# Kernel tuning notes

Hardware: AMD Instinct MI355X
Metric: run time of the kernel (lower is better)

Reference implementation:

```python
import jax, jax.numpy as jnp
import numpy as np

EPS = 1e-6
N_HEADS = 16


def _inner(x, y):
    # Lorentzian inner product: -x0*y0 + <x_space, y_space>
    return -x[..., 0] * y[..., 0] + jnp.sum(x[..., 1:] * y[..., 1:], axis=-1)


def _project(x):
    sp = jnp.clip(x[..., 1:], -8.0, 8.0)
    x0 = jnp.sqrt(1.0 + jnp.sum(sp ** 2, axis=-1, keepdims=True) + EPS)
    return jnp.concatenate([x0, sp], axis=-1)


def _exp_map(x, v):
    vx = _inner(v, x)[..., None]
    v_tan = v + vx * x
    v_ns = jnp.maximum(_inner(v_tan, v_tan), 0.0)
    v_n = jnp.minimum(jnp.sqrt(v_ns + EPS)[..., None], 5.0)
    res = jnp.cosh(v_n) * x + jnp.sinh(v_n) * v_tan / (v_n + EPS)
    return _project(res)


def _log_map(x, y):
    y = _project(y)
    xy = jnp.minimum(_inner(x, y)[..., None], -(1.0 + EPS))
    d = jnp.maximum(jnp.arccosh(jnp.maximum(-xy, 1.0 + EPS)), 0.001)
    direc = y + xy * x
    dn = jnp.sqrt(jnp.maximum(_inner(direc, direc), EPS))[..., None]
    return d * direc / (dn + EPS)


def setup_inputs() -> dict:
    key = jax.random.key(0)
    ks = jax.random.split(key, 5)
    B, T, d = 2, 1024, 1024
    x = jax.random.normal(ks[0], (B, T, d), dtype=jnp.float32)
    s = 0.02
    Wq = jax.random.normal(ks[1], (d, d), dtype=jnp.float32) * s
    Wk = jax.random.normal(ks[2], (d, d), dtype=jnp.float32) * s
    Wv = jax.random.normal(ks[3], (d, d), dtype=jnp.float32) * s
    Wo = jax.random.normal(ks[4], (d, d), dtype=jnp.float32) * s
    return {"x": x, "Wq": Wq, "Wk": Wk, "Wv": Wv, "Wo": Wo}


def reference(x, Wq, Wk, Wv, Wo):
    B, T, d = x.shape
    h = N_HEADS
    dh = d // h
    mu = jnp.zeros((d,), dtype=x.dtype).at[0].set(1.0)  # hyperboloid origin

    v = _log_map(mu, x)  # [B, T, d]

    def proj_h(w):
        hh = w.reshape(B, T, h, dh)
        sp = jnp.clip(hh[..., 1:], -5.0, 5.0)
        x0 = jnp.sqrt(1.0 + jnp.sum(sp ** 2, axis=-1, keepdims=True) + EPS)
        return jnp.transpose(jnp.concatenate([x0, sp], axis=-1), (0, 2, 1, 3))  # [B,h,T,dh]

    q = proj_h(v @ Wq.T)
    k = proj_h(v @ Wk.T)
    vv = jnp.transpose((v @ Wv.T).reshape(B, T, h, dh), (0, 2, 1, 3))  # [B,h,T,dh]

    # Lorentzian scores: -q0*k0 + <q_space, k_space>
    sc = (-jnp.einsum("bhqi,bhki->bhqk", q[..., :1], k[..., :1])
          + jnp.einsum("bhqc,bhkc->bhqk", q[..., 1:], k[..., 1:])) / (dh ** 0.5)
    at = jax.nn.softmax(sc, axis=-1)
    out = jnp.einsum("bhqk,bhkc->bhqc", at, vv)
    out = jnp.transpose(out, (0, 2, 1, 3)).reshape(B, T, d)
    return _project(_exp_map(mu, out @ Wo.T))
```

## Files before the change

### kernel.cpp

```cpp
#include <hip/hip_runtime.h>

#define EPSF 1e-6f

typedef __bf16 bf16x8 __attribute__((ext_vector_type(8)));
typedef float f32x4 __attribute__((ext_vector_type(4)));
typedef __attribute__((address_space(3))) unsigned int as3_uint;
typedef __attribute__((address_space(1))) const unsigned int as1_uint;

__device__ __forceinline__ unsigned short f2bf(float f) {
  unsigned int u = __builtin_bit_cast(unsigned int, f);
  u += 0x7fffu + ((u >> 16) & 1u);
  return (unsigned short)(u >> 16);
}
__device__ __forceinline__ float bf2f(unsigned short u) {
  unsigned int v = (unsigned int)u << 16;
  return __builtin_bit_cast(float, v);
}

__global__ __launch_bounds__(256) void prep_and_conv(
    const float* __restrict__ x, const float* __restrict__ Wq,
    const float* __restrict__ Wk, const float* __restrict__ Wv,
    const float* __restrict__ Wo, unsigned short* __restrict__ vbf,
    unsigned short* __restrict__ wqk, unsigned short* __restrict__ wvb,
    unsigned short* __restrict__ wob) {
  int bid = blockIdx.x;
  int tid = threadIdx.x;
  if (bid >= 2048) {
    int t = bid - 2048;
    int y = t >> 10;
    const float* src = (y == 0) ? Wq : (y == 1) ? Wk : (y == 2) ? Wv : Wo;
    unsigned short* dst = (y == 0) ? wqk : (y == 1) ? wqk + 1048576
                          : (y == 2) ? wvb : wob;
    int i = (t & 1023) * 256 + tid;
    f32x4 v = ((const f32x4*)src)[i];
    ushort4 o;
    o.x = f2bf(v[0]); o.y = f2bf(v[1]); o.z = f2bf(v[2]); o.w = f2bf(v[3]);
    ((ushort4*)dst)[i] = o;
    return;
  }
  int row = bid;
  const float* xr = x + (size_t)row * 1024;
  float vals[4];
  float ssq = 0.f;
#pragma unroll
  for (int i = 0; i < 4; ++i) {
    int c = tid + i * 256;
    float t = xr[c];
    if (c == 0) {
      vals[i] = 0.f;
    } else {
      t = fminf(fmaxf(t, -8.f), 8.f);
      vals[i] = t;
      ssq += t * t;
    }
  }
#pragma unroll
  for (int off = 32; off; off >>= 1) ssq += __shfl_xor(ssq, off);
  __shared__ float red[4];
  int wv = tid >> 6;
  if ((tid & 63) == 0) red[wv] = ssq;
  __syncthreads();
  ssq = red[0] + red[1] + red[2] + red[3];

  float y0 = sqrtf(1.f + ssq + EPSF);
  float xy = fminf(-y0, -(1.f + EPSF));
  float mxy = fmaxf(-xy, 1.f + EPSF);
  float dd = fmaxf(acoshf(mxy), 0.001f);
  float d0 = y0 + xy;
  float inn = ssq - d0 * d0;
  float dn = sqrtf(fmaxf(inn, EPSF));
  float inv = dd / (dn + EPSF);

  unsigned short* vr = vbf + (size_t)row * 1024;
#pragma unroll
  for (int i = 0; i < 4; ++i) {
    int c = tid + i * 256;
    float o = (c == 0) ? d0 * inv : vals[i] * inv;
    vr[c] = f2bf(o);
  }
}

__device__ __forceinline__ void gemm128_dbuf(
    const unsigned short* __restrict__ A, const unsigned short* __restrict__ Bw,
    int K, int row0, int col0, unsigned short* As, unsigned short* Bs,
    f32x4 (*acc)[4]) {
  int tid = threadIdx.x;
  int lane = tid & 63, w = tid >> 6;
  int wm = (w >> 1) * 64, wn = (w & 1) * 64;
  int lq = lane & 15, g = lane >> 4;
  const unsigned short* Ag =
      A + (size_t)(row0 + w * 8 + (lane >> 3)) * K + (lane & 7) * 8;
  const unsigned short* Bg =
      Bw + (size_t)(col0 + w * 8 + (lane >> 3)) * K + (lane & 7) * 8;

  auto stage = [&](int buf, int k0) {
#pragma unroll
    for (int it = 0; it < 4; ++it) {
      __builtin_amdgcn_global_load_lds(
          (as1_uint*)(Ag + (size_t)(it * 32) * K + k0),
          (as3_uint*)&As[buf * 8192 + (it * 32 + w * 8) * 64], 16, 0, 0);
      __builtin_amdgcn_global_load_lds(
          (as1_uint*)(Bg + (size_t)(it * 32) * K + k0),
          (as3_uint*)&Bs[buf * 8192 + (it * 32 + w * 8) * 64], 16, 0, 0);
    }
  };

  stage(0, 0);
  int buf = 0;
  for (int k0 = 0; k0 < K; k0 += 64) {
    __syncthreads();
    if (k0 + 64 < K) stage(buf ^ 1, k0 + 64);
#pragma unroll
    for (int ks = 0; ks < 2; ++ks) {
      bf16x8 af[4], bfr[4];
#pragma unroll
      for (int i = 0; i < 4; ++i)
        af[i] = *(const bf16x8*)&As[buf * 8192 + (wm + i * 16 + lq) * 64 + ks * 32 + g * 8];
#pragma unroll
      for (int j = 0; j < 4; ++j)
        bfr[j] = *(const bf16x8*)&Bs[buf * 8192 + (wn + j * 16 + lq) * 64 + ks * 32 + g * 8];
#pragma unroll
      for (int i = 0; i < 4; ++i)
#pragma unroll
        for (int j = 0; j < 4; ++j)
          acc[i][j] =
              __builtin_amdgcn_mfma_f32_16x16x32_bf16(af[i], bfr[j], acc[i][j], 0, 0, 0);
    }
    buf ^= 1;
  }
}

__global__ __launch_bounds__(256) void gemm_qkv(
    const unsigned short* __restrict__ vbf, const unsigned short* __restrict__ wqk,
    const unsigned short* __restrict__ wvb, unsigned short* __restrict__ qb,
    unsigned short* __restrict__ kb, unsigned short* __restrict__ vtb) {
  __shared__ unsigned short As[2 * 8192];
  __shared__ unsigned short Bs[2 * 8192];
  f32x4 acc[4][4] = {};
  int tid = threadIdx.x;
  int lane = tid & 63, w = tid >> 6;
  int wm = (w >> 1) * 64, wn = (w & 1) * 64;
  int lq = lane & 15, g = lane >> 4;
  int bid = blockIdx.x;
  bool isVt = (bid % 3 == 2);

  if (!isVt) {
    int q = bid - (bid + 1) / 3;
    int row0 = (q & 15) * 128, col0 = (q >> 4) * 128;
    gemm128_dbuf(vbf, wqk, 1024, row0, col0, As, Bs, acc);
    int headg = (col0 + wn) >> 6;
    int qmode = (headg < 16) ? 1 : 0;
    unsigned short* dst = qmode ? qb : kb;
    size_t colb = (size_t)(headg & 15) * 64;
    float scale = qmode ? 0.125f : 1.f;
#pragma unroll
    for (int i = 0; i < 4; ++i)
#pragma unroll
      for (int r = 0; r < 4; ++r) {
        float s = 0.f;
#pragma unroll
        for (int j = 0; j < 4; ++j) {
          float vc = fminf(fmaxf(acc[i][j][r], -5.f), 5.f);
          s += (j == 0 && lq == 0) ? 0.f : vc * vc;
        }
        s += __shfl_xor(s, 1);
        s += __shfl_xor(s, 2);
        s += __shfl_xor(s, 4);
        s += __shfl_xor(s, 8);
        float x0 = sqrtf(1.f + s + EPSF);
        int row = row0 + wm + i * 16 + g * 4 + r;
#pragma unroll
        for (int j = 0; j < 4; ++j) {
          float vc = fminf(fmaxf(acc[i][j][r], -5.f), 5.f);
          float o = (j == 0 && lq == 0) ? (qmode ? -x0 : x0) : vc;
          dst[(size_t)row * 1024 + colb + j * 16 + lq] = f2bf(o * scale);
        }
      }
  } else {
    int t = bid / 3;
    int row0 = (t & 7) * 128, col0 = (t >> 3) * 128;
    gemm128_dbuf(wvb, vbf, 1024, row0, col0, As, Bs, acc);
#pragma unroll
    for (int i = 0; i < 4; ++i)
#pragma unroll
      for (int j = 0; j < 4; ++j)
#pragma unroll
        for (int r = 0; r < 4; ++r)
          vtb[(size_t)(row0 + wm + i * 16 + g * 4 + r) * 2048 + col0 + wn + j * 16 + lq] =
              f2bf(acc[i][j][r]);
  }
}

__global__ __launch_bounds__(256) void gemm_wo(
    const unsigned short* __restrict__ A, const unsigned short* __restrict__ Bw,
    unsigned short* __restrict__ C) {
  __shared__ unsigned short As[2 * 8192];
  __shared__ unsigned short Bs[2 * 4096];
  int tid = threadIdx.x;
  int lane = tid & 63, w = tid >> 6;
  int wm = (w >> 1) * 64, wn = (w & 1) * 32;
  int lq = lane & 15, g = lane >> 4;
  int row0 = (blockIdx.x & 15) * 128, col0 = (blockIdx.x >> 4) * 64;
  f32x4 acc[4][2] = {};
  const unsigned short* Ag =
      A + (size_t)(row0 + w * 8 + (lane >> 3)) * 1024 + (lane & 7) * 8;
  const unsigned short* Bg =
      Bw + (size_t)(col0 + w * 8 + (lane >> 3)) * 1024 + (lane & 7) * 8;

  auto stage = [&](int buf, int k0) {
#pragma unroll
    for (int it = 0; it < 4; ++it)
      __builtin_amdgcn_global_load_lds(
          (as1_uint*)(Ag + (size_t)(it * 32) * 1024 + k0),
          (as3_uint*)&As[buf * 8192 + (it * 32 + w * 8) * 64], 16, 0, 0);
#pragma unroll
    for (int it = 0; it < 2; ++it)
      __builtin_amdgcn_global_load_lds(
          (as1_uint*)(Bg + (size_t)(it * 32) * 1024 + k0),
          (as3_uint*)&Bs[buf * 4096 + (it * 32 + w * 8) * 64], 16, 0, 0);
  };

  stage(0, 0);
  int buf = 0;
  for (int k0 = 0; k0 < 1024; k0 += 64) {
    __syncthreads();
    if (k0 + 64 < 1024) stage(buf ^ 1, k0 + 64);
#pragma unroll
    for (int ks = 0; ks < 2; ++ks) {
      bf16x8 af[4], bfr[2];
#pragma unroll
      for (int i = 0; i < 4; ++i)
        af[i] = *(const bf16x8*)&As[buf * 8192 + (wm + i * 16 + lq) * 64 + ks * 32 + g * 8];
#pragma unroll
      for (int j = 0; j < 2; ++j)
        bfr[j] = *(const bf16x8*)&Bs[buf * 4096 + (wn + j * 16 + lq) * 64 + ks * 32 + g * 8];
#pragma unroll
      for (int i = 0; i < 4; ++i)
#pragma unroll
        for (int j = 0; j < 2; ++j)
          acc[i][j] =
              __builtin_amdgcn_mfma_f32_16x16x32_bf16(af[i], bfr[j], acc[i][j], 0, 0, 0);
    }
    buf ^= 1;
  }
#pragma unroll
  for (int i = 0; i < 4; ++i)
#pragma unroll
    for (int j = 0; j < 2; ++j)
#pragma unroll
      for (int r = 0; r < 4; ++r)
        C[(size_t)(row0 + wm + i * 16 + g * 4 + r) * 1024 + col0 + wn + j * 16 + lq] =
            f2bf(acc[i][j][r]);
}

__global__ __launch_bounds__(256) void attn_mfma(
    const unsigned short* __restrict__ Qb, const unsigned short* __restrict__ Kb,
    const unsigned short* __restrict__ Vtb, unsigned short* __restrict__ Obf) {
  __shared__ unsigned short Ks[2][64 * 64];
  __shared__ unsigned short Vs[2][64 * 64];
  __shared__ unsigned short Ps[4 * 16 * 64];
  int tid = threadIdx.x;
  int lane = tid & 63, w = tid >> 6;
  int g = lane >> 4, lq = lane & 15;
  int bid = blockIdx.x;
  int idx = bid >> 3;
  int bh = (bid & 7) * 4 + (idx & 3);
  int qt = idx >> 2;
  int b = bh >> 4, h = bh & 15;

  const unsigned short* qrow =
      Qb + (size_t)(b * 1024 + qt * 64 + w * 16 + lq) * 1024 + h * 64;
  bf16x8 qf0 = *(const bf16x8*)(qrow + g * 8);
  bf16x8 qf1 = *(const bf16x8*)(qrow + 32 + g * 8);

  float mreg = -1e30f, lreg = 0.f;
  f32x4 acc[4] = {};
  unsigned short* Pw = Ps + w * 16 * 64;
  int sx = 8 * (lq & 7);

  const unsigned short* Ksrc = Kb + (size_t)(b * 1024) * 1024 + h * 64;
  const unsigned short* Vsrc = Vtb + (size_t)(h * 64) * 2048 + b * 1024;

  int srow = lane >> 3;
  int scg = (lane & 7) ^ srow;
  const unsigned short* Kp = Ksrc + (size_t)(w * 8 + srow) * 1024 + scg * 8;
  const unsigned short* Vp = Vsrc + (size_t)(w * 8 + srow) * 2048 + scg * 8;

  auto stage = [&](int buf, int kt) {
#pragma unroll
    for (int it = 0; it < 2; ++it) {
      __builtin_amdgcn_global_load_lds(
          (as1_uint*)(Kp + (size_t)(kt * 64 + it * 32) * 1024),
          (as3_uint*)&Ks[buf][(it * 32 + w * 8) * 64], 16, 0, 0);
      __builtin_amdgcn_global_load_lds(
          (as1_uint*)(Vp + (size_t)(it * 32) * 2048 + kt * 64),
          (as3_uint*)&Vs[buf][(it * 32 + w * 8) * 64], 16, 0, 0);
    }
  };

  auto compute = [&](int buf) {
    f32x4 st[4];
    __builtin_amdgcn_s_setprio(1);
#pragma unroll
    for (int i = 0; i < 4; ++i) {
      int ro = i * 16 + lq;
      int rb = ro * 64, xx = 8 * (ro & 7);
      bf16x8 a0 = *(const bf16x8*)&Ks[buf][rb + ((g * 8) ^ xx)];
      bf16x8 a1 = *(const bf16x8*)&Ks[buf][rb + ((32 + g * 8) ^ xx)];
      f32x4 z = {};
      z = __builtin_amdgcn_mfma_f32_16x16x32_bf16(a0, qf0, z, 0, 0, 0);
      st[i] = __builtin_amdgcn_mfma_f32_16x16x32_bf16(a1, qf1, z, 0, 0, 0);
    }
    __builtin_amdgcn_s_setprio(0);
    float pmax = st[0][0];
#pragma unroll
    for (int i = 0; i < 4; ++i)
#pragma unroll
      for (int r = 0; r < 4; ++r) pmax = fmaxf(pmax, st[i][r]);
    pmax = fmaxf(pmax, __shfl_xor(pmax, 16));
    pmax = fmaxf(pmax, __shfl_xor(pmax, 32));
    if (__any(pmax > mreg + 8.f)) {
      float nm = fmaxf(mreg, pmax);
      float sc_ = __expf(mreg - nm);
      mreg = nm;
      lreg *= sc_;
      float scr[4];
#pragma unroll
      for (int r = 0; r < 4; ++r) scr[r] = __shfl(sc_, g * 4 + r);
#pragma unroll
      for (int jj = 0; jj < 4; ++jj)
#pragma unroll
        for (int r = 0; r < 4; ++r) acc[jj][r] *= scr[r];
    }
    float ps = 0.f;
#pragma unroll
    for (int i = 0; i < 4; ++i) {
      ushort4 pq;
      float p0 = __expf(st[i][0] - mreg);
      float p1 = __expf(st[i][1] - mreg);
      float p2 = __expf(st[i][2] - mreg);
      float p3 = __expf(st[i][3] - mreg);
      ps += (p0 + p1) + (p2 + p3);
      pq.x = f2bf(p0); pq.y = f2bf(p1); pq.z = f2bf(p2); pq.w = f2bf(p3);
      *(ushort4*)&Pw[lq * 64 + ((g * 4 + i * 16) ^ sx)] = pq;
    }
    ps += __shfl_xor(ps, 16);
    ps += __shfl_xor(ps, 32);
    lreg += ps;

    __builtin_amdgcn_s_setprio(1);
#pragma unroll
    for (int ks = 0; ks < 2; ++ks) {
      bf16x8 pa = *(const bf16x8*)&Pw[lq * 64 + ((ks * 32 + g * 8) ^ sx)];
#pragma unroll
      for (int jj = 0; jj < 4; ++jj) {
        int vr = 16 * jj + lq;
        bf16x8 vb = *(const bf16x8*)&Vs[buf][vr * 64 + ((ks * 32 + g * 8) ^ (8 * (vr & 7)))];
        acc[jj] = __builtin_amdgcn_mfma_f32_16x16x32_bf16(pa, vb, acc[jj], 0, 0, 0);
      }
    }
    __builtin_amdgcn_s_setprio(0);
  };

  stage(0, 0);
  int buf = 0;
  for (int kt = 0; kt < 16; ++kt) {
    __syncthreads();
    if (kt + 1 < 16) stage(buf ^ 1, kt + 1);
    compute(buf);
    buf ^= 1;
  }

  float linv = 1.f / lreg;
  float ilr[4];
#pragma unroll
  for (int r = 0; r < 4; ++r) ilr[r] = __shfl(linv, g * 4 + r);
  unsigned short* obase =
      Obf + (size_t)(b * 1024 + qt * 64 + w * 16) * 1024 + h * 64;
#pragma unroll
  for (int r = 0; r < 4; ++r)
#pragma unroll
    for (int jj = 0; jj < 4; ++jj)
      obase[(size_t)(g * 4 + r) * 1024 + 16 * jj + lq] = f2bf(acc[jj][r] * ilr[r]);
}

__global__ __launch_bounds__(256) void expmap_project(
    const unsigned short* __restrict__ c2, float* __restrict__ out) {
  int row = blockIdx.x;
  int tid = threadIdx.x;
  const unsigned short* cr = c2 + (size_t)row * 1024;
  float vals[4];
  float ssq = 0.f;
#pragma unroll
  for (int i = 0; i < 4; ++i) {
    int c = tid + i * 256;
    float t = bf2f(cr[c]);
    vals[i] = (c == 0) ? 0.f : t;
    ssq += vals[i] * vals[i];
  }
#pragma unroll
  for (int off = 32; off; off >>= 1) ssq += __shfl_xor(ssq, off);
  __shared__ float red1[4], red2[4];
  int wv = tid >> 6;
  if ((tid & 63) == 0) red1[wv] = ssq;
  __syncthreads();
  ssq = red1[0] + red1[1] + red1[2] + red1[3];
  float vn = fminf(sqrtf(ssq + EPSF), 5.f);
  float bf = sinhf(vn) / (vn + EPSF);
  float s2 = 0.f;
#pragma unroll
  for (int i = 0; i < 4; ++i) {
    float r = fminf(fmaxf(bf * vals[i], -8.f), 8.f);
    vals[i] = r;
    s2 += r * r;
  }
#pragma unroll
  for (int off = 32; off; off >>= 1) s2 += __shfl_xor(s2, off);
  if ((tid & 63) == 0) red2[wv] = s2;
  __syncthreads();
  s2 = red2[0] + red2[1] + red2[2] + red2[3];
  float x0 = sqrtf(1.f + s2 + EPSF);
  float* orow = out + (size_t)row * 1024;
#pragma unroll
  for (int i = 0; i < 4; ++i) {
    int c = tid + i * 256;
    orow[c] = (c == 0) ? x0 : vals[i];
  }
}

extern "C" void kernel_launch(void* const* d_in, const int* in_sizes, int n_in,
                              void* d_out, int out_size, void* d_ws, size_t ws_size,
                              hipStream_t stream) {
  (void)in_sizes; (void)n_in; (void)out_size; (void)ws_size;
  const float* x  = (const float*)d_in[0];
  const float* Wq = (const float*)d_in[1];
  const float* Wk = (const float*)d_in[2];
  const float* Wv = (const float*)d_in[3];
  const float* Wo = (const float*)d_in[4];
  float* out = (float*)d_out;

  char* w = (char*)d_ws;
  unsigned short* vbf = (unsigned short*)w; w += (size_t)2048 * 1024 * 2;
  unsigned short* wqk = (unsigned short*)w; w += (size_t)2048 * 1024 * 2;
  unsigned short* wvb = (unsigned short*)w; w += (size_t)1024 * 1024 * 2;
  unsigned short* wob = (unsigned short*)w; w += (size_t)1024 * 1024 * 2;
  unsigned short* vtb = (unsigned short*)w; w += (size_t)1024 * 2048 * 2;
  unsigned short* qb  = (unsigned short*)w; w += (size_t)2048 * 1024 * 2;
  unsigned short* kb  = (unsigned short*)w; w += (size_t)2048 * 1024 * 2;
  unsigned short* aob = (unsigned short*)w; w += (size_t)2048 * 1024 * 2;
  unsigned short* c2  = (unsigned short*)w; w += (size_t)2048 * 1024 * 2;

  prep_and_conv<<<6144, 256, 0, stream>>>(x, Wq, Wk, Wv, Wo, vbf, wqk, wvb, wob);

  gemm_qkv<<<384, 256, 0, stream>>>(vbf, wqk, wvb, qb, kb, vtb);

  attn_mfma<<<512, 256, 0, stream>>>(qb, kb, vtb, aob);

  gemm_wo<<<256, 256, 0, stream>>>(aob, wob, c2);
  expmap_project<<<2048, 256, 0, stream>>>(c2, out);
}
```

Measured before the change: 84.20 us.

## Rebalance QKV GEMM V-tiles and double attention query tile per block

Measured after the change: 85.83 us. No clear change (+1.9%).

```diff
diff --git a/kernel.cpp b/kernel.cpp
--- a/kernel.cpp
+++ b/kernel.cpp
@@ -136,16 +136,15 @@
     unsigned short* __restrict__ kb, unsigned short* __restrict__ vtb) {
   __shared__ unsigned short As[2 * 8192];
   __shared__ unsigned short Bs[2 * 8192];
-  f32x4 acc[4][4] = {};
   int tid = threadIdx.x;
   int lane = tid & 63, w = tid >> 6;
-  int wm = (w >> 1) * 64, wn = (w & 1) * 64;
   int lq = lane & 15, g = lane >> 4;
   int bid = blockIdx.x;
-  bool isVt = (bid % 3 == 2);
-
-  if (!isVt) {
-    int q = bid - (bid + 1) / 3;
+
+  if ((bid & 1) == 0) {
+    int q = bid >> 1;
+    int wm = (w >> 1) * 64, wn = (w & 1) * 64;
+    f32x4 acc[4][4] = {};
     int row0 = (q & 15) * 128, col0 = (q >> 4) * 128;
     gemm128_dbuf(vbf, wqk, 1024, row0, col0, As, Bs, acc);
     int headg = (col0 + wn) >> 6;
@@ -177,13 +176,53 @@
         }
       }
   } else {
-    int t = bid / 3;
-    int row0 = (t & 7) * 128, col0 = (t >> 3) * 128;
-    gemm128_dbuf(wvb, vbf, 1024, row0, col0, As, Bs, acc);
+    int t = bid >> 1;
+    int wm = (w >> 1) * 64, wn = (w & 1) * 32;
+    int row0 = (t & 7) * 128, col0 = (t >> 3) * 64;
+    f32x4 acc[4][2] = {};
+    const unsigned short* Ag =
+        wvb + (size_t)(row0 + w * 8 + (lane >> 3)) * 1024 + (lane & 7) * 8;
+    const unsigned short* Bg =
+        vbf + (size_t)(col0 + w * 8 + (lane >> 3)) * 1024 + (lane & 7) * 8;
+    auto stage = [&](int buf, int k0) {
+#pragma unroll
+      for (int it = 0; it < 4; ++it)
+        __builtin_amdgcn_global_load_lds(
+            (as1_uint*)(Ag + (size_t)(it * 32) * 1024 + k0),
+            (as3_uint*)&As[buf * 8192 + (it * 32 + w * 8) * 64], 16, 0, 0);
+#pragma unroll
+      for (int it = 0; it < 2; ++it)
+        __builtin_amdgcn_global_load_lds(
+            (as1_uint*)(Bg + (size_t)(it * 32) * 1024 + k0),
+            (as3_uint*)&Bs[buf * 4096 + (it * 32 + w * 8) * 64], 16, 0, 0);
+    };
+    stage(0, 0);
+    int buf = 0;
+    for (int k0 = 0; k0 < 1024; k0 += 64) {
+      __syncthreads();
+      if (k0 + 64 < 1024) stage(buf ^ 1, k0 + 64);
+#pragma unroll
+      for (int ks = 0; ks < 2; ++ks) {
+        bf16x8 af[4], bfr[2];
+#pragma unroll
+        for (int i = 0; i < 4; ++i)
+          af[i] = *(const bf16x8*)&As[buf * 8192 + (wm + i * 16 + lq) * 64 + ks * 32 + g * 8];
+#pragma unroll
+        for (int j = 0; j < 2; ++j)
+          bfr[j] = *(const bf16x8*)&Bs[buf * 4096 + (wn + j * 16 + lq) * 64 + ks * 32 + g * 8];
+#pragma unroll
+        for (int i = 0; i < 4; ++i)
+#pragma unroll
+          for (int j = 0; j < 2; ++j)
+            acc[i][j] =
+                __builtin_amdgcn_mfma_f32_16x16x32_bf16(af[i], bfr[j], acc[i][j], 0, 0, 0);
+      }
+      buf ^= 1;
+    }
 #pragma unroll
     for (int i = 0; i < 4; ++i)
 #pragma unroll
-      for (int j = 0; j < 4; ++j)
+      for (int j = 0; j < 2; ++j)
 #pragma unroll
         for (int r = 0; r < 4; ++r)
           vtb[(size_t)(row0 + wm + i * 16 + g * 4 + r) * 2048 + col0 + wn + j * 16 + lq] =
@@ -253,12 +292,12 @@
             f2bf(acc[i][j][r]);
 }
 
-__global__ __launch_bounds__(256) void attn_mfma(
+__global__ __launch_bounds__(512) void attn_mfma(
     const unsigned short* __restrict__ Qb, const unsigned short* __restrict__ Kb,
     const unsigned short* __restrict__ Vtb, unsigned short* __restrict__ Obf) {
   __shared__ unsigned short Ks[2][64 * 64];
   __shared__ unsigned short Vs[2][64 * 64];
-  __shared__ unsigned short Ps[4 * 16 * 64];
+  __shared__ unsigned short Ps[8 * 16 * 64];
   int tid = threadIdx.x;
   int lane = tid & 63, w = tid >> 6;
   int g = lane >> 4, lq = lane & 15;
@@ -269,7 +308,7 @@
   int b = bh >> 4, h = bh & 15;
 
   const unsigned short* qrow =
-      Qb + (size_t)(b * 1024 + qt * 64 + w * 16 + lq) * 1024 + h * 64;
+      Qb + (size_t)(b * 1024 + qt * 128 + w * 16 + lq) * 1024 + h * 64;
   bf16x8 qf0 = *(const bf16x8*)(qrow + g * 8);
   bf16x8 qf1 = *(const bf16x8*)(qrow + 32 + g * 8);
 
@@ -287,15 +326,12 @@
   const unsigned short* Vp = Vsrc + (size_t)(w * 8 + srow) * 2048 + scg * 8;
 
   auto stage = [&](int buf, int kt) {
-#pragma unroll
-    for (int it = 0; it < 2; ++it) {
-      __builtin_amdgcn_global_load_lds(
-          (as1_uint*)(Kp + (size_t)(kt * 64 + it * 32) * 1024),
-          (as3_uint*)&Ks[buf][(it * 32 + w * 8) * 64], 16, 0, 0);
-      __builtin_amdgcn_global_load_lds(
-          (as1_uint*)(Vp + (size_t)(it * 32) * 2048 + kt * 64),
-          (as3_uint*)&Vs[buf][(it * 32 + w * 8) * 64], 16, 0, 0);
-    }
+    __builtin_amdgcn_global_load_lds(
+        (as1_uint*)(Kp + (size_t)(kt * 64) * 1024),
+        (as3_uint*)&Ks[buf][(w * 8) * 64], 16, 0, 0);
+    __builtin_amdgcn_global_load_lds(
+        (as1_uint*)(Vp + kt * 64),
+        (as3_uint*)&Vs[buf][(w * 8) * 64], 16, 0, 0);
   };
 
   auto compute = [&](int buf) {
@@ -376,7 +412,7 @@
 #pragma unroll
   for (int r = 0; r < 4; ++r) ilr[r] = __shfl(linv, g * 4 + r);
   unsigned short* obase =
-      Obf + (size_t)(b * 1024 + qt * 64 + w * 16) * 1024 + h * 64;
+      Obf + (size_t)(b * 1024 + qt * 128 + w * 16) * 1024 + h * 64;
 #pragma unroll
   for (int r = 0; r < 4; ++r)
 #pragma unroll
@@ -452,9 +488,9 @@
 
   prep_and_conv<<<6144, 256, 0, stream>>>(x, Wq, Wk, Wv, Wo, vbf, wqk, wvb, wob);
 
-  gemm_qkv<<<384, 256, 0, stream>>>(vbf, wqk, wvb, qb, kb, vtb);
-
-  attn_mfma<<<512, 256, 0, stream>>>(qb, kb, vtb, aob);
+  gemm_qkv<<<512, 256, 0, stream>>>(vbf, wqk, wvb, qb, kb, vtb);
+
+  attn_mfma<<<256, 512, 0, stream>>>(qb, kb, vtb, aob);
 
   gemm_wo<<<256, 256, 0, stream>>>(aob, wob, c2);
   expmap_project<<<2048, 256, 0, stream>>>(c2, out);
```
